# Performance work log

Measured on AMD Instinct MI355X. Metric: run time of the kernel, lower is better.

The kernel has to match this reference:

```python
import jax, jax.numpy as jnp
import numpy as np

N_BASE = 4          # len('NACGT'[1:])
STATE_LEN = 5
S = N_BASE ** STATE_LEN   # 1024 states
NZ = N_BASE + 1           # 5 transitions per state
T_STEPS = 800
BATCH = 32


def _build_idx():
    # idx[i] = [i, 0*256 + i//4, 1*256 + i//4, 2*256 + i//4, 3*256 + i//4]
    i = np.arange(S)
    trans = np.stack([j * (S // N_BASE) + i // N_BASE for j in range(N_BASE)], axis=1)
    idx = np.concatenate([i[:, None], trans], axis=1).astype(np.int64)      # (S, NZ)
    # transposed transition structure (stable sort: duplicates grouped deterministically)
    idx_T = np.argsort(idx.ravel(), kind='stable').reshape(S, NZ)
    idx_T_div = idx_T // NZ
    return jnp.asarray(idx), jnp.asarray(idx_T), jnp.asarray(idx_T_div)


def _scan(Ms, idx, v0):
    """Log-semiring recurrence: alpha[t+1] = logsumexp(Ms[t] + alpha[t][:, idx], -1).
    Ms: (T, N, S, NZ); idx: (S, NZ); v0: (N, S). Returns (T+1, N, S)."""
    def step(alpha, M):
        nxt = jax.scipy.special.logsumexp(M + alpha[:, idx], axis=-1)  # (N, S)
        return nxt, nxt
    _, alphas = jax.lax.scan(step, v0, Ms)
    return jnp.concatenate([v0[None], alphas], axis=0)


def setup_inputs() -> dict:
    key = jax.random.key(0)
    scores = jax.random.normal(key, (T_STEPS, BATCH, S * NZ), dtype=jnp.float32)
    return {"scores": scores}


def reference(scores):
    idx, idx_T, idx_T_div = _build_idx()
    T, N, _ = scores.shape
    Ms = scores.reshape(T, N, S, NZ)
    v0 = jnp.zeros((N, S), scores.dtype)   # semiring Log.one == 0.0
    # forward scores
    fwd = _scan(Ms, idx, v0)                                   # (T+1, N, S)
    # backward scores: gather transposed transitions, run scan in reverse time
    Ms_T = scores[:, :, idx_T]                                 # (T, N, S, NZ)
    bwd = jnp.flip(_scan(jnp.flip(Ms_T, 0), idx_T_div, v0), 0)  # (T+1, N, S)
    posts = jax.nn.softmax(fwd + bwd, axis=-1)                 # (T+1, N, S)
    return (jnp.swapaxes(scores, 0, 1),
            jnp.swapaxes(bwd, 0, 1),
            jnp.swapaxes(posts, 0, 1))
```

## Files before the change

kernel.cpp:

```cpp
#include <hip/hip_runtime.h>

#define T_STEPS 800
#define NBATCH  32
#define SSTATES 1024
#define ROW     5120

struct ScanSmem {
  float sbuf[2][ROW];
  float abuf[2][SSTATES];
};

__device__ __forceinline__ float lse5(float v0, float v1, float v2, float v3, float v4) {
  float m = fmaxf(fmaxf(fmaxf(v0, v1), fmaxf(v2, v3)), v4);
  float s = __expf(v0 - m) + __expf(v1 - m) + __expf(v2 - m) +
            __expf(v3 - m) + __expf(v4 - m);
  return m + __logf(s);
}

__device__ __forceinline__ void sync_lds() {
  asm volatile("s_waitcnt lgkmcnt(0)" ::: "memory");
  __builtin_amdgcn_s_barrier();
  asm volatile("" ::: "memory");
}

template <int DIR>
__device__ void scan_run(const float* __restrict__ scores, float* __restrict__ out,
                         float* __restrict__ out0, int n, ScanSmem& sm) {
  const int tid = threadIdx.x;
  const float* base = scores + (size_t)n * ROW;
  float* outn = out + (size_t)n * (T_STEPS + 1) * SSTATES;

  sm.abuf[0][tid] = 0.0f;
  float a = 0.0f;
  if (DIR == 0) outn[tid] = 0.0f;
  else          outn[(size_t)T_STEPS * SSTATES + tid] = 0.0f;

  const int sc0 = 5 * tid;
  int q, sc1;
  if (DIR == 0) {
    q = tid >> 2;
    sc1 = 0;
  } else {
    const int j = tid >> 8;
    q = tid & 255;
    sc1 = 20 * q + 1 + j;
  }

  float r[4][5];
#pragma unroll
  for (int i = 0; i < 4; ++i) {
    const int t = DIR ? (T_STEPS - 1 - i) : i;
    const float* rp = base + (size_t)t * (NBATCH * ROW);
#pragma unroll
    for (int k = 0; k < 5; ++k) r[i][k] = rp[tid + k * SSTATES];
  }

  for (int p = 0; p < T_STEPS; p += 4) {
#pragma unroll
    for (int i = 0; i < 4; ++i) {
      const int step = p + i;
      const int t = DIR ? (T_STEPS - 1 - step) : step;
      const int cur = i & 1;

#pragma unroll
      for (int k = 0; k < 5; ++k) sm.sbuf[cur][tid + k * SSTATES] = r[i][k];

      if (step < 400) {
        float* o0 = out0 + ((size_t)n * T_STEPS + t) * ROW;
#pragma unroll
        for (int k = 0; k < 5; ++k) o0[tid + k * SSTATES] = r[i][k];
      }

      sync_lds();

      if (step + 4 < T_STEPS) {
        const int tn = DIR ? (T_STEPS - 1 - (step + 4)) : (step + 4);
        const float* rp = base + (size_t)tn * (NBATCH * ROW);
#pragma unroll
        for (int k = 0; k < 5; ++k) r[i][k] = rp[tid + k * SSTATES];
      }

      float na;
      if (DIR == 0) {
        const float v0 = sm.sbuf[cur][sc0 + 0] + a;
        const float v1 = sm.sbuf[cur][sc0 + 1] + sm.abuf[cur][q];
        const float v2 = sm.sbuf[cur][sc0 + 2] + sm.abuf[cur][q + 256];
        const float v3 = sm.sbuf[cur][sc0 + 3] + sm.abuf[cur][q + 512];
        const float v4 = sm.sbuf[cur][sc0 + 4] + sm.abuf[cur][q + 768];
        na = lse5(v0, v1, v2, v3, v4);
      } else {
        const float4 av = *(const float4*)&sm.abuf[cur][4 * q];
        const float v0 = sm.sbuf[cur][sc0]      + a;
        const float v1 = sm.sbuf[cur][sc1 + 0]  + av.x;
        const float v2 = sm.sbuf[cur][sc1 + 5]  + av.y;
        const float v3 = sm.sbuf[cur][sc1 + 10] + av.z;
        const float v4 = sm.sbuf[cur][sc1 + 15] + av.w;
        na = lse5(v0, v1, v2, v3, v4);
      }

      const size_t t_out = DIR ? (size_t)t : (size_t)(step + 1);
      outn[t_out * SSTATES + tid] = na;
      a = na;
      sm.abuf[cur ^ 1][tid] = na;
    }
  }
}

__global__ __launch_bounds__(1024) void fused_scan(const float* __restrict__ scores,
                                                   float* __restrict__ out0,
                                                   float* __restrict__ bwdo,
                                                   float* __restrict__ fposts) {
  __shared__ ScanSmem sm;
  const int b = blockIdx.x;
  if (b < NBATCH) scan_run<0>(scores, fposts, out0, b, sm);
  else            scan_run<1>(scores, bwdo,   out0, b - NBATCH, sm);
}

__global__ __launch_bounds__(256) void posts_kernel(float* __restrict__ fp,
                                                    const float* __restrict__ bp) {
  const int lane = threadIdx.x & 63;
  const int wid  = threadIdx.x >> 6;
  const size_t row = (size_t)blockIdx.x * 4 + wid;
  float* f = fp + row * SSTATES;
  const float* b = bp + row * SSTATES;

  float x[16];
#pragma unroll
  for (int k = 0; k < 4; ++k) {
    const float4 fv = ((const float4*)f)[lane + 64 * k];
    const float4 bv = ((const float4*)b)[lane + 64 * k];
    x[4 * k + 0] = fv.x + bv.x;
    x[4 * k + 1] = fv.y + bv.y;
    x[4 * k + 2] = fv.z + bv.z;
    x[4 * k + 3] = fv.w + bv.w;
  }
  float m = x[0];
#pragma unroll
  for (int j = 1; j < 16; ++j) m = fmaxf(m, x[j]);
#pragma unroll
  for (int off = 32; off >= 1; off >>= 1) m = fmaxf(m, __shfl_xor(m, off));
  float ssum = 0.0f;
#pragma unroll
  for (int j = 0; j < 16; ++j) { x[j] = __expf(x[j] - m); ssum += x[j]; }
#pragma unroll
  for (int off = 32; off >= 1; off >>= 1) ssum += __shfl_xor(ssum, off);
  const float inv = 1.0f / ssum;
#pragma unroll
  for (int k = 0; k < 4; ++k) {
    float4 o;
    o.x = x[4 * k + 0] * inv;
    o.y = x[4 * k + 1] * inv;
    o.z = x[4 * k + 2] * inv;
    o.w = x[4 * k + 3] * inv;
    ((float4*)f)[lane + 64 * k] = o;
  }
}

extern "C" void kernel_launch(void* const* d_in, const int* in_sizes, int n_in,
                              void* d_out, int out_size, void* d_ws, size_t ws_size,
                              hipStream_t stream) {
  (void)in_sizes; (void)n_in; (void)d_ws; (void)ws_size; (void)out_size;
  const float* scores = (const float*)d_in[0];
  float* out = (float*)d_out;
  float* out0   = out;
  float* bwdo   = out + (size_t)NBATCH * T_STEPS * ROW;
  float* fposts = bwdo + (size_t)NBATCH * (T_STEPS + 1) * SSTATES;

  fused_scan<<<64, 1024, 0, stream>>>(scores, out0, bwdo, fposts);
  posts_kernel<<<(NBATCH * (T_STEPS + 1)) / 4, 256, 0, stream>>>(fposts, bwdo);
}
```

Before: 830.8 us.

## Shrink scan blocks to 256 threads with register-resident scores and separate copy blocks

```diff
diff --git a/kernel.cpp b/kernel.cpp
--- a/kernel.cpp
+++ b/kernel.cpp
@@ -2,13 +2,12 @@
 
 #define T_STEPS 800
 #define NBATCH  32
-#define SSTATES 1024
+#define SST     1024
 #define ROW     5120
 
-struct ScanSmem {
-  float sbuf[2][ROW];
-  float abuf[2][SSTATES];
-};
+#define SCAN_BLOCKS 64
+#define COPY_BLOCKS 1536
+#define GRID (SCAN_BLOCKS + COPY_BLOCKS)
 
 __device__ __forceinline__ float lse5(float v0, float v1, float v2, float v3, float v4) {
   float m = fmaxf(fmaxf(fmaxf(v0, v1), fmaxf(v2, v3)), v4);
@@ -24,96 +23,120 @@
 }
 
 template <int DIR>
+__device__ __forceinline__ void prefetch(const float* __restrict__ base, int step, int u,
+                                         float* __restrict__ r, float* __restrict__ s) {
+  const int t = DIR ? (T_STEPS - 1 - step) : step;
+  const float* rp = base + (size_t)t * (NBATCH * ROW);
+#pragma unroll
+  for (int m = 0; m < 5; ++m)
+    *(float4*)&r[4 * m] = *(const float4*)&rp[20 * u + 4 * m];
+  if (DIR) {
+#pragma unroll
+    for (int j = 0; j < 4; ++j) s[j] = rp[5 * u + 1280 * j];
+  }
+}
+
+template <int DIR>
 __device__ void scan_run(const float* __restrict__ scores, float* __restrict__ out,
-                         float* __restrict__ out0, int n, ScanSmem& sm) {
-  const int tid = threadIdx.x;
+                         int n, float (*abuf)[SST]) {
+  const int u = threadIdx.x;
   const float* base = scores + (size_t)n * ROW;
-  float* outn = out + (size_t)n * (T_STEPS + 1) * SSTATES;
+  float* outn = out + (size_t)n * (T_STEPS + 1) * SST;
 
-  sm.abuf[0][tid] = 0.0f;
-  float a = 0.0f;
-  if (DIR == 0) outn[tid] = 0.0f;
-  else          outn[(size_t)T_STEPS * SSTATES + tid] = 0.0f;
+  float a[4] = {0.f, 0.f, 0.f, 0.f};
 
-  const int sc0 = 5 * tid;
-  int q, sc1;
-  if (DIR == 0) {
-    q = tid >> 2;
-    sc1 = 0;
-  } else {
-    const int j = tid >> 8;
-    q = tid & 255;
-    sc1 = 20 * q + 1 + j;
+  float v[4][20];
+  float s5[4][4];
+#pragma unroll
+  for (int i = 0; i < 4; ++i) prefetch<DIR>(base, i, u, v[i], s5[i]);
+
+  abuf[0][u] = 0.f; abuf[0][u + 256] = 0.f; abuf[0][u + 512] = 0.f; abuf[0][u + 768] = 0.f;
+  {
+    const float4 z = {0.f, 0.f, 0.f, 0.f};
+    const size_t t0 = DIR ? (size_t)T_STEPS : 0;
+    ((float4*)(outn + t0 * SST))[u] = z;
   }
-
-  float r[4][5];
-#pragma unroll
-  for (int i = 0; i < 4; ++i) {
-    const int t = DIR ? (T_STEPS - 1 - i) : i;
-    const float* rp = base + (size_t)t * (NBATCH * ROW);
-#pragma unroll
-    for (int k = 0; k < 5; ++k) r[i][k] = rp[tid + k * SSTATES];
-  }
+  sync_lds();
 
   for (int p = 0; p < T_STEPS; p += 4) {
 #pragma unroll
     for (int i = 0; i < 4; ++i) {
       const int step = p + i;
-      const int t = DIR ? (T_STEPS - 1 - step) : step;
-      const int cur = i & 1;
+      const int cur = step & 1;
+      const int nxt = cur ^ 1;
 
-#pragma unroll
-      for (int k = 0; k < 5; ++k) sm.sbuf[cur][tid + k * SSTATES] = r[i][k];
-
-      if (step < 400) {
-        float* o0 = out0 + ((size_t)n * T_STEPS + t) * ROW;
-#pragma unroll
-        for (int k = 0; k < 5; ++k) o0[tid + k * SSTATES] = r[i][k];
+      float4 pv;
+      if (DIR == 0) {
+        pv.x = abuf[cur][u];
+        pv.y = abuf[cur][u + 256];
+        pv.z = abuf[cur][u + 512];
+        pv.w = abuf[cur][u + 768];
+      } else {
+        pv = *(const float4*)&abuf[cur][4 * u];
       }
 
-      sync_lds();
-
-      if (step + 4 < T_STEPS) {
-        const int tn = DIR ? (T_STEPS - 1 - (step + 4)) : (step + 4);
-        const float* rp = base + (size_t)tn * (NBATCH * ROW);
+      float na[4];
 #pragma unroll
-        for (int k = 0; k < 5; ++k) r[i][k] = rp[tid + k * SSTATES];
+      for (int j = 0; j < 4; ++j) {
+        float v0, v1, v2, v3, v4;
+        if (DIR == 0) {
+          v0 = v[i][5 * j + 0] + a[j];
+          v1 = v[i][5 * j + 1] + pv.x;
+          v2 = v[i][5 * j + 2] + pv.y;
+          v3 = v[i][5 * j + 3] + pv.z;
+          v4 = v[i][5 * j + 4] + pv.w;
+        } else {
+          v0 = s5[i][j]          + a[j];
+          v1 = v[i][1 + j + 0]   + pv.x;
+          v2 = v[i][1 + j + 5]   + pv.y;
+          v3 = v[i][1 + j + 10]  + pv.z;
+          v4 = v[i][1 + j + 15]  + pv.w;
+        }
+        na[j] = lse5(v0, v1, v2, v3, v4);
       }
 
-      float na;
+      if (step + 4 < T_STEPS) prefetch<DIR>(base, step + 4, u, v[i], s5[i]);
+
       if (DIR == 0) {
-        const float v0 = sm.sbuf[cur][sc0 + 0] + a;
-        const float v1 = sm.sbuf[cur][sc0 + 1] + sm.abuf[cur][q];
-        const float v2 = sm.sbuf[cur][sc0 + 2] + sm.abuf[cur][q + 256];
-        const float v3 = sm.sbuf[cur][sc0 + 3] + sm.abuf[cur][q + 512];
-        const float v4 = sm.sbuf[cur][sc0 + 4] + sm.abuf[cur][q + 768];
-        na = lse5(v0, v1, v2, v3, v4);
+        const float4 o = {na[0], na[1], na[2], na[3]};
+        ((float4*)(outn + (size_t)(step + 1) * SST))[u] = o;
+        *(float4*)&abuf[nxt][4 * u] = o;
       } else {
-        const float4 av = *(const float4*)&sm.abuf[cur][4 * q];
-        const float v0 = sm.sbuf[cur][sc0]      + a;
-        const float v1 = sm.sbuf[cur][sc1 + 0]  + av.x;
-        const float v2 = sm.sbuf[cur][sc1 + 5]  + av.y;
-        const float v3 = sm.sbuf[cur][sc1 + 10] + av.z;
-        const float v4 = sm.sbuf[cur][sc1 + 15] + av.w;
-        na = lse5(v0, v1, v2, v3, v4);
+        const int t = T_STEPS - 1 - step;
+#pragma unroll
+        for (int j = 0; j < 4; ++j) {
+          outn[(size_t)t * SST + u + 256 * j] = na[j];
+          abuf[nxt][u + 256 * j] = na[j];
+        }
       }
+#pragma unroll
+      for (int j = 0; j < 4; ++j) a[j] = na[j];
 
-      const size_t t_out = DIR ? (size_t)t : (size_t)(step + 1);
-      outn[t_out * SSTATES + tid] = na;
-      a = na;
-      sm.abuf[cur ^ 1][tid] = na;
+      sync_lds();
     }
   }
 }
 
-__global__ __launch_bounds__(1024) void fused_scan(const float* __restrict__ scores,
-                                                   float* __restrict__ out0,
-                                                   float* __restrict__ bwdo,
-                                                   float* __restrict__ fposts) {
-  __shared__ ScanSmem sm;
+__global__ __launch_bounds__(256) void mega(const float* __restrict__ scores,
+                                            float* __restrict__ out0,
+                                            float* __restrict__ bwdo,
+                                            float* __restrict__ fposts) {
+  __shared__ float abuf[2][SST];
   const int b = blockIdx.x;
-  if (b < NBATCH) scan_run<0>(scores, fposts, out0, b, sm);
-  else            scan_run<1>(scores, bwdo,   out0, b - NBATCH, sm);
+  if (b < SCAN_BLOCKS) {
+    if (b < NBATCH) scan_run<0>(scores, fposts, b, abuf);
+    else            scan_run<1>(scores, bwdo,   b - NBATCH, abuf);
+  } else {
+    const int tb = b - SCAN_BLOCKS;
+    for (int r = tb; r < NBATCH * T_STEPS; r += COPY_BLOCKS) {
+      const int t = r / NBATCH, n = r % NBATCH;
+      const float4* src = (const float4*)(scores + (size_t)r * ROW);
+      float4* dst = (float4*)(out0 + ((size_t)n * T_STEPS + t) * ROW);
+#pragma unroll
+      for (int i = 0; i < 5; ++i)
+        dst[threadIdx.x + 256 * i] = src[threadIdx.x + 256 * i];
+    }
+  }
 }
 
 __global__ __launch_bounds__(256) void posts_kernel(float* __restrict__ fp,
@@ -121,8 +144,8 @@
   const int lane = threadIdx.x & 63;
   const int wid  = threadIdx.x >> 6;
   const size_t row = (size_t)blockIdx.x * 4 + wid;
-  float* f = fp + row * SSTATES;
-  const float* b = bp + row * SSTATES;
+  float* f = fp + row * SST;
+  const float* b = bp + row * SST;
 
   float x[16];
 #pragma unroll
@@ -164,8 +187,8 @@
   float* out = (float*)d_out;
   float* out0   = out;
   float* bwdo   = out + (size_t)NBATCH * T_STEPS * ROW;
-  float* fposts = bwdo + (size_t)NBATCH * (T_STEPS + 1) * SSTATES;
+  float* fposts = bwdo + (size_t)NBATCH * (T_STEPS + 1) * SST;
 
-  fused_scan<<<64, 1024, 0, stream>>>(scores, out0, bwdo, fposts);
+  mega<<<GRID, 256, 0, stream>>>(scores, out0, bwdo, fposts);
   posts_kernel<<<(NBATCH * (T_STEPS + 1)) / 4, 256, 0, stream>>>(fposts, bwdo);
 }
```

After: 833.8 us. No clear change (+0.4%).
